# Kernel tuning notes

Measured on AMD Instinct MI355X. Metric: run time of the kernel, lower is better.

Reference implementation:

```python
import jax, jax.numpy as jnp
import numpy as np

D_MODEL = 512
NUM_HEADS = 8
HEAD_DIM = D_MODEL // NUM_HEADS
BATCH = 4
SEQ = 2048
NEG_INF = -1e9  # large negative instead of -inf so fully-masked rows stay finite


def setup_inputs() -> dict:
    key = jax.random.key(0)
    k1, k2, k3, k4 = jax.random.split(key, 4)
    x = jax.random.normal(k1, (BATCH, SEQ, D_MODEL), dtype=jnp.float32)
    mask = jnp.zeros((1, 1, SEQ, SEQ), dtype=jnp.float32)  # unused: paded_mask path taken
    paded_mask = jax.random.randint(k2, (BATCH, SEQ), 0, 2).astype(bool)
    W_qkv = jax.random.normal(k3, (D_MODEL, 3 * D_MODEL), dtype=jnp.float32) * (D_MODEL ** -0.5)
    W_out = jax.random.normal(k4, (D_MODEL, D_MODEL), dtype=jnp.float32) * (D_MODEL ** -0.5)
    return {"x": x, "mask": mask, "paded_mask": paded_mask, "W_qkv": W_qkv, "W_out": W_out}


def reference(x, mask, paded_mask, W_qkv, W_out):
    B, S, D = x.shape
    H, hd = NUM_HEADS, HEAD_DIM
    qkv = x @ W_qkv                                   # [B,S,3D]
    # Faithful to original: reshape (NOT transpose) (B,S,H,3hd) -> (B,H,S,3hd)
    qkv = qkv.reshape(B, S, H, 3 * hd).reshape(B, H, S, 3 * hd)
    q, k, v = jnp.split(qkv, 3, axis=3)               # each [B,H,S,hd]
    scaled = jnp.einsum("bhqd,bhkd->bhqk", q, k) / (hd ** 0.5)
    valid = paded_mask.astype(scaled.dtype)           # [B,S]
    # masked_padding_Decoder: softmax over valid keys for valid query rows,
    # zeros on invalid rows and invalid columns.
    logits = jnp.where(paded_mask[:, None, None, :], scaled, NEG_INF)
    att = jax.nn.softmax(logits, axis=-1)
    att = att * valid[:, None, :, None] * valid[:, None, None, :]
    values = jnp.einsum("bhqk,bhkd->bhqd", att, v)    # [B,H,S,hd]
    # Faithful to original: plain reshape (B,H,S,hd) -> (B,S,D)
    values = values.reshape(B, S, H * hd)
    return values @ W_out
```

## Files before the change

kernel.cpp:

```cpp
#include <hip/hip_runtime.h>
#include <hip/hip_bf16.h>
#include <math.h>
#include <stdint.h>

#define BATCH   4
#define SEQ     2048
#define DMODEL  512
#define NHEADS  8
#define HDIM    64
#define QKV_N   (3*DMODEL)

typedef short bf8  __attribute__((ext_vector_type(8)));
typedef float f32x4 __attribute__((ext_vector_type(4)));

#define MFMA16(a,b,c) __builtin_amdgcn_mfma_f32_16x16x32_bf16((a),(b),(c),0,0,0)

__device__ inline unsigned short f2bf(float f){
  unsigned int u = __float_as_uint(f);
  u += 0x7FFFu + ((u >> 16) & 1u);
  return (unsigned short)(u >> 16);
}

__device__ inline unsigned int pack_bf2(float a, float b){
  __hip_bfloat162 h = __float22bfloat162_rn(make_float2(a, b));
  return *reinterpret_cast<unsigned int*>(&h);
}

__device__ __forceinline__ float exp2_hw(float x){
#if defined(__has_builtin)
#if __has_builtin(__builtin_amdgcn_exp2f)
  return __builtin_amdgcn_exp2f(x);
#else
  float r; asm("v_exp_f32 %0, %1" : "=v"(r) : "v"(x)); return r;
#endif
#else
  float r; asm("v_exp_f32 %0, %1" : "=v"(r) : "v"(x)); return r;
#endif
}

__device__ __forceinline__ void gload_lds16(const unsigned short* g,
                                            unsigned short* l){
  __builtin_amdgcn_global_load_lds(
      (const __attribute__((address_space(1))) unsigned int*)g,
      (__attribute__((address_space(3))) unsigned int*)l,
      16, 0, 0);
}

__global__ __launch_bounds__(256) void prep(
    const float* __restrict__ x, const float* __restrict__ Wqkv,
    const float* __restrict__ Wout, const int* __restrict__ pmask,
    unsigned short* __restrict__ Xh, unsigned short* __restrict__ WqkvT,
    unsigned short* __restrict__ WoutT, int* __restrict__ Idx,
    int* __restrict__ Cnt, unsigned short* __restrict__ Ob)
{
  __shared__ unsigned short Ts[64][72];
  __shared__ int ps[256];
  __shared__ int tot;
  const int t = threadIdx.x;
  const int bx = blockIdx.x;
  if (bx < 2048) {
    const int i = bx*256 + t;
    const float4 a = reinterpret_cast<const float4*>(x)[2*i];
    const float4 b = reinterpret_cast<const float4*>(x)[2*i+1];
    uint4 o; unsigned short* us = reinterpret_cast<unsigned short*>(&o);
    us[0]=f2bf(a.x); us[1]=f2bf(a.y); us[2]=f2bf(a.z); us[3]=f2bf(a.w);
    us[4]=f2bf(b.x); us[5]=f2bf(b.y); us[6]=f2bf(b.z); us[7]=f2bf(b.w);
    reinterpret_cast<uint4*>(Xh)[i] = o;
    return;
  }
  if (bx >= 2308) {
    const int g = (bx - 2308)*256 + t;
    uint4 z = {0u,0u,0u,0u};
    uint4* p = reinterpret_cast<uint4*>(Ob) + (size_t)g*4;
    p[0]=z; p[1]=z; p[2]=z; p[3]=z;
    return;
  }
  if (bx >= 2304) {
    const int b = bx - 2304;
    const int* mb = pmask + b*SEQ;
    int loc[8]; int c = 0; const int base = t*8;
#pragma unroll
    for (int j=0;j<8;++j){ const int v = (mb[base+j] != 0); loc[j]=v; c+=v; }
    ps[t] = c; __syncthreads();
    for (int off=1; off<256; off<<=1){
      const int v = (t>=off) ? ps[t-off] : 0;
      __syncthreads(); ps[t] += v; __syncthreads();
    }
    int excl = ps[t] - c;
#pragma unroll
    for (int j=0;j<8;++j) if (loc[j]) Idx[b*SEQ + (excl++)] = base + j;
    if (t == 255){ Cnt[b] = ps[255]; tot = ps[255]; }
    __syncthreads();
    for (int k = tot + t; k < SEQ; k += 256) Idx[b*SEQ + k] = 0;
    return;
  }
  const float* in; unsigned short* out; int R, C, gx, gy;
  if (bx < 2048 + 192) {
    const int bid = bx - 2048;
    gx = bid % 24; gy = bid / 24; in = Wqkv; out = WqkvT; R = DMODEL; C = QKV_N;
  } else {
    const int bid = bx - 2240;
    gx = bid % 8;  gy = bid / 8;  in = Wout; out = WoutT; R = DMODEL; C = DMODEL;
  }
  const int r0 = gy<<6, c0 = gx<<6;
  const int rr = t>>2, cs = (t&3)<<4;
#pragma unroll
  for (int p=0;p<4;++p){
    float4 v = *reinterpret_cast<const float4*>(in + (size_t)(r0+rr)*C + c0 + cs + p*4);
    Ts[rr][cs+p*4+0]=f2bf(v.x); Ts[rr][cs+p*4+1]=f2bf(v.y);
    Ts[rr][cs+p*4+2]=f2bf(v.z); Ts[rr][cs+p*4+3]=f2bf(v.w);
  }
  __syncthreads();
  const int cc = t>>2, rs = (t&3)<<4;
#pragma unroll
  for (int p=0;p<4;++p){
    ushort4 o;
    o.x = Ts[rs+p*4+0][cc]; o.y = Ts[rs+p*4+1][cc];
    o.z = Ts[rs+p*4+2][cc]; o.w = Ts[rs+p*4+3][cc];
    *reinterpret_cast<ushort4*>(out + (size_t)(c0+cc)*R + r0 + rs + p*4) = o;
  }
}

__global__ __launch_bounds__(256) void gemm_qkv_mfma(
    const unsigned short* __restrict__ A, const unsigned short* __restrict__ Bt,
    unsigned short* __restrict__ QKV)
{
  __shared__ unsigned short As[128][64];
  __shared__ unsigned short Bs[128][64];
  const int t = threadIdx.x;
  const int w = t>>6, lane = t&63, quad = lane>>4, l15 = lane&15;
  const int wr = (w>>1)<<6, wc = (w&1)<<6;
  const int linear = blockIdx.y*12 + blockIdx.x;
  const int swz = (linear & 7)*96 + (linear >> 3);
  const int m0 = (swz/12)<<7, n0 = (swz%12)<<7;
  const int row = t>>3, seg = t&7;
  const unsigned short* Agp = A  + (size_t)(m0+row)*DMODEL + seg*8;
  const unsigned short* Bgp = Bt + (size_t)(n0+row)*DMODEL + seg*8;
  f32x4 acc[4][4];
#pragma unroll
  for (int i=0;i<4;++i)
#pragma unroll
    for (int j=0;j<4;++j) acc[i][j] = (f32x4){0.f,0.f,0.f,0.f};

  for (int k0=0;k0<DMODEL;k0+=64){
    __syncthreads();
#pragma unroll
    for (int p=0;p<4;++p){
      gload_lds16(Agp + (size_t)p*32*DMODEL + k0, &As[(w<<3)+(p<<5)][0]);
      gload_lds16(Bgp + (size_t)p*32*DMODEL + k0, &Bs[(w<<3)+(p<<5)][0]);
    }
    __syncthreads();
#pragma unroll
    for (int ks=0;ks<2;++ks){
      bf8 af[4], bfr[4];
#pragma unroll
      for (int mi=0;mi<4;++mi)
        af[mi]  = *reinterpret_cast<const bf8*>(&As[wr+mi*16+l15][ks*32+quad*8]);
#pragma unroll
      for (int nj=0;nj<4;++nj)
        bfr[nj] = *reinterpret_cast<const bf8*>(&Bs[wc+(l15<<2)+nj][ks*32+quad*8]);
#pragma unroll
      for (int mi=0;mi<4;++mi)
#pragma unroll
        for (int nj=0;nj<4;++nj) acc[mi][nj] = MFMA16(af[mi], bfr[nj], acc[mi][nj]);
    }
  }
  const int cbase = n0 + wc + (l15<<2);
  bool isq[4];
#pragma unroll
  for (int nj=0;nj<4;++nj) isq[nj] = ((cbase+nj) % 192) < 64;
#pragma unroll
  for (int mi=0;mi<4;++mi)
#pragma unroll
    for (int i=0;i<4;++i){
      const int m = m0 + wr + mi*16 + quad*4 + i;
      unsigned long long pk = 0;
#pragma unroll
      for (int nj=0;nj<4;++nj){
        float v = acc[mi][nj][i];
        if (isq[nj]) v *= 0.18033688f;
        pk |= (unsigned long long)f2bf(v) << (16*nj);
      }
      *reinterpret_cast<unsigned long long*>(QKV + (size_t)m*QKV_N + cbase) = pk;
    }
}

__global__ __launch_bounds__(256) void v_transpose(
    const unsigned short* __restrict__ QKV, const int* __restrict__ Idx,
    const int* __restrict__ Cnt, unsigned short* __restrict__ VT)
{
  __shared__ unsigned short Td[64][76];
  const int t = threadIdx.x;
  const int bh = blockIdx.y, b = bh>>3, hp = bh&7;
  const int s0 = blockIdx.x<<6;
  if (s0 >= ((Cnt[b] + 63) & ~63)) return;
  const size_t rbase = (size_t)(b*SEQ + hp*256);
  const int sr = t>>2, db = (t&3)<<4;
  const int s = Idx[b*SEQ + s0 + sr];
  const unsigned short* vp =
      QKV + (rbase + (s>>3))*QKV_N + (s&7)*192 + 128 + db;
  uint4 a = *reinterpret_cast<const uint4*>(vp);
  uint4 c = *reinterpret_cast<const uint4*>(vp + 8);
  const unsigned short* ua = reinterpret_cast<const unsigned short*>(&a);
  const unsigned short* uc = reinterpret_cast<const unsigned short*>(&c);
#pragma unroll
  for (int j=0;j<8;++j) Td[db+j][sr]   = ua[j];
#pragma unroll
  for (int j=0;j<8;++j) Td[db+8+j][sr] = uc[j];
  __syncthreads();
  const int L = t&15, d0 = t>>4;
  unsigned short* Op = VT + (size_t)bh*HDIM*SEQ + s0 + (L<<2);
#pragma unroll
  for (int cc=0;cc<4;++cc){
    const int d = d0 + (cc<<4);
    *reinterpret_cast<unsigned long long*>(Op + (size_t)d*SEQ) =
        *reinterpret_cast<const unsigned long long*>(&Td[d][L<<2]);
  }
}

__global__ __launch_bounds__(512, 4) void attn_mfma(
    const unsigned short* __restrict__ QKV, const unsigned short* __restrict__ VT,
    const int* __restrict__ Idx, const int* __restrict__ Cnt,
    unsigned short* __restrict__ O)
{
  __shared__ unsigned short Ks[2][64][72];
  __shared__ unsigned short Vs[2][64][72];
  __shared__ unsigned short Pl[8][16][72];
  const int t = threadIdx.x;
  const int w = t>>6, lane = t&63, quad = lane>>4, l15 = lane&15;
  const int linear = blockIdx.y*16 + blockIdx.x;
  const int swz = (linear & 7)*64 + (linear >> 3);
  const int bh = swz >> 4, b = bh>>3, hp = bh&7;
  const int q0 = (swz & 15) << 7;
  const int kcnt = Cnt[b];
  const int kend = (kcnt + 63) & ~63;
  if (q0 >= kend) return;
  const int qs = q0 + (w<<4);
  const int* Idxb = Idx + b*SEQ;
  const f32x4 Z4 = {0.f,0.f,0.f,0.f};

  const size_t rbase = (size_t)(b*SEQ + hp*256);
  bf8 qf[2];
  {
    const int sq = Idxb[qs + l15];
    const unsigned short* qp =
        QKV + (rbase + (sq>>3))*QKV_N + (sq&7)*192 + (quad<<3);
    qf[0] = *reinterpret_cast<const bf8*>(qp);
    qf[1] = *reinterpret_cast<const bf8*>(qp + 32);
  }
  const unsigned short* Vg = VT + (size_t)bh*HDIM*SEQ;

  bf8 ones;
#pragma unroll
  for (int j=0;j<8;++j) ones[j] = (short)0x3F80;

  const int srow = t>>3, sc8 = (t&7)<<3;
  const int krow = ((srow&3)<<4) + (srow>>2);

  f32x4 of[4]; f32x4 lsv = Z4;
#pragma unroll
  for (int i=0;i<4;++i) of[i]=Z4;

  uint4 gk0, gv0;
  {
    const int s = Idxb[srow];
    const unsigned short* kp =
        QKV + (rbase + (s>>3))*QKV_N + (s&7)*192 + 64 + sc8;
    gk0 = *reinterpret_cast<const uint4*>(kp);
    gv0 = *reinterpret_cast<const uint4*>(Vg + (size_t)srow*SEQ + sc8);
  }
  *reinterpret_cast<uint4*>(&Ks[0][krow][sc8]) = gk0;
  *reinterpret_cast<uint4*>(&Vs[0][srow][sc8]) = gv0;
  {
    const int s = Idxb[64 + srow];
    const unsigned short* kp =
        QKV + (rbase + (s>>3))*QKV_N + (s&7)*192 + 64 + sc8;
    gk0 = *reinterpret_cast<const uint4*>(kp);
    gv0 = *reinterpret_cast<const uint4*>(Vg + (size_t)srow*SEQ + 64 + sc8);
  }
  __syncthreads();

  auto iter = [&](unsigned short (&KSC)[64][72], unsigned short (&VSC)[64][72],
                  unsigned short (&KSN)[64][72], unsigned short (&VSN)[64][72],
                  int kt) {
    if (kt + 64 < kend){
      *reinterpret_cast<uint4*>(&KSN[krow][sc8]) = gk0;
      *reinterpret_cast<uint4*>(&VSN[srow][sc8]) = gv0;
    }
    if (kt + 128 < kend){
      const int s = Idxb[kt + 128 + srow];
      const unsigned short* kp =
          QKV + (rbase + (s>>3))*QKV_N + (s&7)*192 + 64 + sc8;
      gk0 = *reinterpret_cast<const uint4*>(kp);
      gv0 = *reinterpret_cast<const uint4*>(
          Vg + (size_t)srow*SEQ + (kt + 128) + sc8);
    }

    bf8 kf[4][2];
#pragma unroll
    for (int nf=0;nf<4;++nf){
      kf[nf][0] = *reinterpret_cast<const bf8*>(&KSC[nf*16+l15][quad<<3]);
      kf[nf][1] = *reinterpret_cast<const bf8*>(&KSC[nf*16+l15][32+(quad<<3)]);
    }

    f32x4 sc[4];
    __builtin_amdgcn_s_setprio(1);
#pragma unroll
    for (int nf=0;nf<4;++nf){
      f32x4 s = MFMA16(qf[0], kf[nf][0], Z4);
      sc[nf] = MFMA16(qf[1], kf[nf][1], s);
    }
    __builtin_amdgcn_s_setprio(0);
    const int kbase = kt + (l15<<2);
    float pv[4][4];
#pragma unroll
    for (int nf=0;nf<4;++nf){
      const bool on = (kbase + nf) < kcnt;
#pragma unroll
      for (int i=0;i<4;++i)
        pv[nf][i] = on ? exp2_hw(sc[nf][i]) : 0.f;
    }
#pragma unroll
    for (int i=0;i<4;++i){
      const unsigned int lo = pack_bf2(pv[0][i], pv[1][i]);
      const unsigned int hi = pack_bf2(pv[2][i], pv[3][i]);
      *reinterpret_cast<unsigned long long*>(&Pl[w][(quad<<2)+i][l15<<2]) =
          ((unsigned long long)hi<<32) | lo;
    }

    bf8 pa[2];
    pa[0] = *reinterpret_cast<const bf8*>(&Pl[w][l15][quad<<3]);
    pa[1] = *reinterpret_cast<const bf8*>(&Pl[w][l15][32+(quad<<3)]);
    __builtin_amdgcn_s_setprio(1);
    {
      f32x4 l = MFMA16(pa[0], ones, lsv);
      lsv = MFMA16(pa[1], ones, l);
    }
#pragma unroll
    for (int nf=0;nf<4;++nf){
      const bf8 v0 = *reinterpret_cast<const bf8*>(&VSC[nf*16+l15][quad<<3]);
      const bf8 v1 = *reinterpret_cast<const bf8*>(&VSC[nf*16+l15][32+(quad<<3)]);
      f32x4 o = MFMA16(pa[0], v0, of[nf]);
      of[nf] = MFMA16(pa[1], v1, o);
    }
    __builtin_amdgcn_s_setprio(0);
    __syncthreads();
  };

  for (int kt=0; kt<kend; kt+=128){
    iter(Ks[0], Vs[0], Ks[1], Vs[1], kt);
    if (kt + 64 < kend)
      iter(Ks[1], Vs[1], Ks[0], Vs[0], kt+64);
  }

  unsigned short* Op = O + (size_t)bh*SEQ*HDIM;
#pragma unroll
  for (int i=0;i<4;++i){
    const int q = qs + (quad<<2) + i;
    if (q < kcnt){
      const int orig = Idxb[q];
      const float l = lsv[i];
      const float inv = (l > 0.f) ? 1.f/l : 0.f;
#pragma unroll
      for (int nf=0;nf<4;++nf)
        Op[(size_t)orig*HDIM + (nf<<4) + l15] = f2bf(of[nf][i]*inv);
    }
  }
}

__global__ __launch_bounds__(256) void gemm_out_mfma(
    const unsigned short* __restrict__ A, const unsigned short* __restrict__ Bt,
    float* __restrict__ Out)
{
  __shared__ unsigned short As[128][64];
  __shared__ unsigned short Bs[64][64];
  const int t = threadIdx.x;
  const int w = t>>6, lane = t&63, quad = lane>>4, l15 = lane&15;
  const int wr = (w>>1)<<6, wc = (w&1)<<5;
  const int linear = blockIdx.y*8 + blockIdx.x;
  const int swz = (linear & 7)*64 + (linear >> 3);
  const int m0 = (swz>>3)<<7, n0 = (swz&7)<<6;
  const int row = t>>3, seg = t&7;
  const unsigned short* Agp = A  + (size_t)(m0+row)*DMODEL + seg*8;
  const unsigned short* Bgp = Bt + (size_t)(n0+row)*DMODEL + seg*8;
  f32x4 acc[4][2];
#pragma unroll
  for (int i=0;i<4;++i)
#pragma unroll
    for (int j=0;j<2;++j) acc[i][j] = (f32x4){0.f,0.f,0.f,0.f};

  for (int k0=0;k0<DMODEL;k0+=64){
    __syncthreads();
#pragma unroll
    for (int p=0;p<4;++p)
      gload_lds16(Agp + (size_t)p*32*DMODEL + k0, &As[(w<<3)+(p<<5)][0]);
#pragma unroll
    for (int p=0;p<2;++p)
      gload_lds16(Bgp + (size_t)p*32*DMODEL + k0, &Bs[(w<<3)+(p<<5)][0]);
    __syncthreads();
#pragma unroll
    for (int ks=0;ks<2;++ks){
      bf8 af[4], bfr[2];
#pragma unroll
      for (int mi=0;mi<4;++mi)
        af[mi]  = *reinterpret_cast<const bf8*>(&As[wr+mi*16+l15][ks*32+quad*8]);
#pragma unroll
      for (int nj=0;nj<2;++nj)
        bfr[nj] = *reinterpret_cast<const bf8*>(&Bs[wc+(l15<<1)+nj][ks*32+quad*8]);
#pragma unroll
      for (int mi=0;mi<4;++mi)
#pragma unroll
        for (int nj=0;nj<2;++nj) acc[mi][nj] = MFMA16(af[mi], bfr[nj], acc[mi][nj]);
    }
  }
  const int cbase = n0 + wc + (l15<<1);
#pragma unroll
  for (int mi=0;mi<4;++mi)
#pragma unroll
    for (int i=0;i<4;++i){
      const int m = m0 + wr + mi*16 + quad*4 + i;
      const float2 o = make_float2(acc[mi][0][i], acc[mi][1][i]);
      *reinterpret_cast<float2*>(Out + (size_t)m*DMODEL + cbase) = o;
    }
}

extern "C" void kernel_launch(void* const* d_in, const int* in_sizes, int n_in,
                              void* d_out, int out_size, void* d_ws, size_t ws_size,
                              hipStream_t stream) {
  (void)in_sizes; (void)n_in; (void)out_size; (void)ws_size;
  const float* x     = (const float*)d_in[0];
  const int*   pmask = (const int*)d_in[2];
  const float* Wqkv  = (const float*)d_in[3];
  const float* Wout  = (const float*)d_in[4];
  float* out = (float*)d_out;

  const size_t per = (size_t)BATCH*NHEADS*SEQ*HDIM;
  unsigned short* Xh    = (unsigned short*)d_ws;
  unsigned short* WqkvT = Xh    + (size_t)8192*512;
  unsigned short* WoutT = WqkvT + (size_t)1536*512;
  unsigned short* QKVb  = WoutT + (size_t)512*512;
  unsigned short* VbT   = QKVb  + (size_t)8192*QKV_N;
  unsigned short* Ob    = VbT + per;
  int* Idx = (int*)(Ob + per);
  int* Cnt = Idx + (size_t)BATCH*SEQ;

  prep<<<2820, 256, 0, stream>>>(x, Wqkv, Wout, pmask, Xh, WqkvT, WoutT,
                                 Idx, Cnt, Ob);
  gemm_qkv_mfma<<<dim3(QKV_N/128, 8192/128), 256, 0, stream>>>(Xh, WqkvT, QKVb);
  v_transpose<<<dim3(SEQ/64, BATCH*NHEADS), 256, 0, stream>>>(
      QKVb, Idx, Cnt, VbT);
  attn_mfma<<<dim3(SEQ/128, BATCH*NHEADS), 512, 0, stream>>>(
      QKVb, VbT, Idx, Cnt, Ob);
  gemm_out_mfma<<<dim3(DMODEL/64, 8192/128), 256, 0, stream>>>(Ob, WoutT, out);
}
```

Before: 170.2 us.

## Register-prefetch GEMM tiles with padded, row-permuted LDS instead of direct LDS loads

Both projection GEMMs now stage global tiles through registers and prefetch the next K-slice while the current slice's MFMAs run, replacing the direct global-to-LDS loads. The LDS tiles gain 8 elements of row padding to avoid bank conflicts on the fragment reads. B rows are permuted when stored so that fragment reads become contiguous per lane while the epilogue column mapping stays the same. This costs extra registers and an extra LDS write pass per slice, in exchange for overlapping global latency with compute.

Measured after the change: 219.9 us. 1.29x slower.

```diff
diff --git a/kernel.cpp b/kernel.cpp
--- a/kernel.cpp
+++ b/kernel.cpp
@@ -36,14 +36,6 @@
 #else
   float r; asm("v_exp_f32 %0, %1" : "=v"(r) : "v"(x)); return r;
 #endif
-}
-
-__device__ __forceinline__ void gload_lds16(const unsigned short* g,
-                                            unsigned short* l){
-  __builtin_amdgcn_global_load_lds(
-      (const __attribute__((address_space(1))) unsigned int*)g,
-      (__attribute__((address_space(3))) unsigned int*)l,
-      16, 0, 0);
 }
 
 __global__ __launch_bounds__(256) void prep(
@@ -125,8 +117,8 @@
     const unsigned short* __restrict__ A, const unsigned short* __restrict__ Bt,
     unsigned short* __restrict__ QKV)
 {
-  __shared__ unsigned short As[128][64];
-  __shared__ unsigned short Bs[128][64];
+  __shared__ unsigned short As[128][72];
+  __shared__ unsigned short Bs[128][72];
   const int t = threadIdx.x;
   const int w = t>>6, lane = t&63, quad = lane>>4, l15 = lane&15;
   const int wr = (w>>1)<<6, wc = (w&1)<<6;
@@ -136,20 +128,38 @@
   const int row = t>>3, seg = t&7;
   const unsigned short* Agp = A  + (size_t)(m0+row)*DMODEL + seg*8;
   const unsigned short* Bgp = Bt + (size_t)(n0+row)*DMODEL + seg*8;
+  int wrB[4];
+#pragma unroll
+  for (int p=0;p<4;++p){
+    const int m = row + (p<<5);
+    wrB[p] = (m & 64) | ((m & 3) << 4) | ((m & 63) >> 2);
+  }
   f32x4 acc[4][4];
 #pragma unroll
   for (int i=0;i<4;++i)
 #pragma unroll
     for (int j=0;j<4;++j) acc[i][j] = (f32x4){0.f,0.f,0.f,0.f};
 
+  uint4 ga[4], gb[4];
+#pragma unroll
+  for (int p=0;p<4;++p){
+    ga[p] = *reinterpret_cast<const uint4*>(Agp + (size_t)p*32*DMODEL);
+    gb[p] = *reinterpret_cast<const uint4*>(Bgp + (size_t)p*32*DMODEL);
+  }
   for (int k0=0;k0<DMODEL;k0+=64){
-    __syncthreads();
 #pragma unroll
     for (int p=0;p<4;++p){
-      gload_lds16(Agp + (size_t)p*32*DMODEL + k0, &As[(w<<3)+(p<<5)][0]);
-      gload_lds16(Bgp + (size_t)p*32*DMODEL + k0, &Bs[(w<<3)+(p<<5)][0]);
-    }
-    __syncthreads();
+      *reinterpret_cast<uint4*>(&As[row+(p<<5)][seg*8]) = ga[p];
+      *reinterpret_cast<uint4*>(&Bs[wrB[p]][seg*8])     = gb[p];
+    }
+    __syncthreads();
+    if (k0 + 64 < DMODEL){
+#pragma unroll
+      for (int p=0;p<4;++p){
+        ga[p] = *reinterpret_cast<const uint4*>(Agp + (size_t)p*32*DMODEL + k0 + 64);
+        gb[p] = *reinterpret_cast<const uint4*>(Bgp + (size_t)p*32*DMODEL + k0 + 64);
+      }
+    }
 #pragma unroll
     for (int ks=0;ks<2;++ks){
       bf8 af[4], bfr[4];
@@ -158,12 +168,13 @@
         af[mi]  = *reinterpret_cast<const bf8*>(&As[wr+mi*16+l15][ks*32+quad*8]);
 #pragma unroll
       for (int nj=0;nj<4;++nj)
-        bfr[nj] = *reinterpret_cast<const bf8*>(&Bs[wc+(l15<<2)+nj][ks*32+quad*8]);
+        bfr[nj] = *reinterpret_cast<const bf8*>(&Bs[wc+(nj<<4)+l15][ks*32+quad*8]);
 #pragma unroll
       for (int mi=0;mi<4;++mi)
 #pragma unroll
         for (int nj=0;nj<4;++nj) acc[mi][nj] = MFMA16(af[mi], bfr[nj], acc[mi][nj]);
     }
+    __syncthreads();
   }
   const int cbase = n0 + wc + (l15<<2);
   bool isq[4];
@@ -372,8 +383,8 @@
     const unsigned short* __restrict__ A, const unsigned short* __restrict__ Bt,
     float* __restrict__ Out)
 {
-  __shared__ unsigned short As[128][64];
-  __shared__ unsigned short Bs[64][64];
+  __shared__ unsigned short As[128][72];
+  __shared__ unsigned short Bs[64][72];
   const int t = threadIdx.x;
   const int w = t>>6, lane = t&63, quad = lane>>4, l15 = lane&15;
   const int wr = (w>>1)<<6, wc = (w&1)<<5;
@@ -383,21 +394,42 @@
   const int row = t>>3, seg = t&7;
   const unsigned short* Agp = A  + (size_t)(m0+row)*DMODEL + seg*8;
   const unsigned short* Bgp = Bt + (size_t)(n0+row)*DMODEL + seg*8;
+  int wrB[2];
+#pragma unroll
+  for (int p=0;p<2;++p){
+    const int m = row + (p<<5);
+    wrB[p] = (m & 32) | ((m & 1) << 4) | ((m & 31) >> 1);
+  }
   f32x4 acc[4][2];
 #pragma unroll
   for (int i=0;i<4;++i)
 #pragma unroll
     for (int j=0;j<2;++j) acc[i][j] = (f32x4){0.f,0.f,0.f,0.f};
 
+  uint4 ga[4], gb[2];
+#pragma unroll
+  for (int p=0;p<4;++p)
+    ga[p] = *reinterpret_cast<const uint4*>(Agp + (size_t)p*32*DMODEL);
+#pragma unroll
+  for (int p=0;p<2;++p)
+    gb[p] = *reinterpret_cast<const uint4*>(Bgp + (size_t)p*32*DMODEL);
+
   for (int k0=0;k0<DMODEL;k0+=64){
-    __syncthreads();
 #pragma unroll
     for (int p=0;p<4;++p)
-      gload_lds16(Agp + (size_t)p*32*DMODEL + k0, &As[(w<<3)+(p<<5)][0]);
+      *reinterpret_cast<uint4*>(&As[row+(p<<5)][seg*8]) = ga[p];
 #pragma unroll
     for (int p=0;p<2;++p)
-      gload_lds16(Bgp + (size_t)p*32*DMODEL + k0, &Bs[(w<<3)+(p<<5)][0]);
-    __syncthreads();
+      *reinterpret_cast<uint4*>(&Bs[wrB[p]][seg*8]) = gb[p];
+    __syncthreads();
+    if (k0 + 64 < DMODEL){
+#pragma unroll
+      for (int p=0;p<4;++p)
+        ga[p] = *reinterpret_cast<const uint4*>(Agp + (size_t)p*32*DMODEL + k0 + 64);
+#pragma unroll
+      for (int p=0;p<2;++p)
+        gb[p] = *reinterpret_cast<const uint4*>(Bgp + (size_t)p*32*DMODEL + k0 + 64);
+    }
 #pragma unroll
     for (int ks=0;ks<2;++ks){
       bf8 af[4], bfr[2];
@@ -406,12 +438,13 @@
         af[mi]  = *reinterpret_cast<const bf8*>(&As[wr+mi*16+l15][ks*32+quad*8]);
 #pragma unroll
       for (int nj=0;nj<2;++nj)
-        bfr[nj] = *reinterpret_cast<const bf8*>(&Bs[wc+(l15<<1)+nj][ks*32+quad*8]);
+        bfr[nj] = *reinterpret_cast<const bf8*>(&Bs[wc+(nj<<4)+l15][ks*32+quad*8]);
 #pragma unroll
       for (int mi=0;mi<4;++mi)
 #pragma unroll
         for (int nj=0;nj<2;++nj) acc[mi][nj] = MFMA16(af[mi], bfr[nj], acc[mi][nj]);
     }
+    __syncthreads();
   }
   const int cbase = n0 + wc + (l15<<1);
 #pragma unroll
```
